# Kernel optimization log

Hardware: AMD Instinct MI355X
Metric: run time of the kernel (lower is better)

The kernel has to match this reference:

```python
import jax, jax.numpy as jnp
import numpy as np

X, Y, Z = 300, 300, 300
C = 16
N = 1048576
SCALE = 0.1


def _bilinear_sample(img, grid):
    # img: (C, H, W); grid: (M, 2) with (x, y) in [-1, 1]; align_corners=True
    _, H, W = img.shape
    ix = (grid[:, 0] + 1.0) * 0.5 * (W - 1)
    iy = (grid[:, 1] + 1.0) * 0.5 * (H - 1)
    ix0f = jnp.floor(ix)
    iy0f = jnp.floor(iy)
    wx = ix - ix0f  # (M,)
    wy = iy - iy0f
    ix0 = jnp.clip(ix0f.astype(jnp.int32), 0, W - 1)
    ix1 = jnp.clip(ix0 + 1, 0, W - 1)
    iy0 = jnp.clip(iy0f.astype(jnp.int32), 0, H - 1)
    iy1 = jnp.clip(iy0 + 1, 0, H - 1)
    # gathers give (C, M)
    v00 = img[:, iy0, ix0]
    v01 = img[:, iy0, ix1]
    v10 = img[:, iy1, ix0]
    v11 = img[:, iy1, ix1]
    return (v00 * (1 - wx) * (1 - wy) + v01 * wx * (1 - wy)
            + v10 * (1 - wx) * wy + v11 * wx * wy)  # (C, M)


def setup_inputs() -> dict:
    key = jax.random.key(0)
    ks = jax.random.split(key, 8)
    coords_plane = jax.random.uniform(ks[0], (3, 1, N, 1, 2), jnp.float32) * 2.0 - 1.0
    coords_line = jax.random.uniform(ks[1], (3, 1, N, 1, 2), jnp.float32) * 2.0 - 1.0
    plane_xy = SCALE * jax.random.normal(ks[2], (1, C, Y, X), jnp.float32)
    plane_yz = SCALE * jax.random.normal(ks[3], (1, C, Z, Y), jnp.float32)
    plane_xz = SCALE * jax.random.normal(ks[4], (1, C, Z, X), jnp.float32)
    line_x = SCALE * jax.random.normal(ks[5], (1, C, X, 1), jnp.float32)
    line_y = SCALE * jax.random.normal(ks[6], (1, C, Y, 1), jnp.float32)
    line_z = SCALE * jax.random.normal(ks[7], (1, C, Z, 1), jnp.float32)
    return {"coords_plane": coords_plane, "coords_line": coords_line,
            "plane_xy": plane_xy, "plane_yz": plane_yz, "plane_xz": plane_xz,
            "line_x": line_x, "line_y": line_y, "line_z": line_z}


def reference(coords_plane, coords_line, plane_xy, plane_yz, plane_xz,
              line_x, line_y, line_z):
    # coords_*[i]: (1, N, 1, 2) -> flatten to (N, 2)
    cp = coords_plane.reshape(3, -1, 2)
    cl = coords_line.reshape(3, -1, 2)
    f_xy = _bilinear_sample(plane_xy[0], cp[0])  # (C, N)
    f_yz = _bilinear_sample(plane_yz[0], cp[1])
    f_xz = _bilinear_sample(plane_xz[0], cp[2])
    f_x = _bilinear_sample(line_x[0], cl[0])
    f_y = _bilinear_sample(line_y[0], cl[1])
    f_z = _bilinear_sample(line_z[0], cl[2])
    out_x = (f_yz * f_x).T  # (N, C)
    out_y = (f_xz * f_y).T
    out_z = (f_xy * f_z).T
    return (out_x, out_y, out_z)
```

## Files before the change

kernel.cpp:

```cpp
#include <hip/hip_runtime.h>

#define DIMSZ 300
#define CCH   16
#define NPTS  1048576

typedef _Float16 half4 __attribute__((ext_vector_type(4)));
typedef float    fvec4 __attribute__((ext_vector_type(4)));
typedef float    fvec2 __attribute__((ext_vector_type(2)));

__device__ __forceinline__ fvec4 h2f(half4 h) {
    fvec4 r;
    r.x = (float)h[0]; r.y = (float)h[1]; r.z = (float)h[2]; r.w = (float)h[3];
    return r;
}

__global__ __launch_bounds__(256) void transpose_planes(
    const float* __restrict__ a, const float* __restrict__ b, const float* __restrict__ c,
    _Float16* __restrict__ ta, _Float16* __restrict__ tb, _Float16* __restrict__ tc)
{
    const int HW = DIMSZ * DIMSZ;
    const float* in  = (blockIdx.y == 0) ? a  : (blockIdx.y == 1) ? b  : c;
    _Float16*    out = (blockIdx.y == 0) ? ta : (blockIdx.y == 1) ? tb : tc;

    __shared__ float tile[64][CCH + 1];
    int pix0 = blockIdx.x * 64;
    int t = threadIdx.x;

    int p  = t & 63;
    int cg = t >> 6;
#pragma unroll
    for (int k = 0; k < 4; ++k) {
        int ch  = cg * 4 + k;
        int pix = pix0 + p;
        tile[p][ch] = (pix < HW) ? __builtin_nontemporal_load(&in[(size_t)ch * HW + pix]) : 0.f;
    }
    __syncthreads();

    int q  = t & 3;
    int pr = t >> 2;
    int pix = pix0 + pr;
    if (pix < HW) {
        half4 h;
        h[0] = (_Float16)tile[pr][q * 4 + 0];
        h[1] = (_Float16)tile[pr][q * 4 + 1];
        h[2] = (_Float16)tile[pr][q * 4 + 2];
        h[3] = (_Float16)tile[pr][q * 4 + 3];
        ((half4*)out)[(size_t)pix * 4 + q] = h;
    }
}

__global__ __launch_bounds__(256) void transpose_lines(
    const float* __restrict__ a, const float* __restrict__ b, const float* __restrict__ c,
    float* __restrict__ ta, float* __restrict__ tb, float* __restrict__ tc)
{
    const float* in  = (blockIdx.y == 0) ? a  : (blockIdx.y == 1) ? b  : c;
    float*       out = (blockIdx.y == 0) ? ta : (blockIdx.y == 1) ? tb : tc;
    for (int idx = threadIdx.x; idx < DIMSZ * CCH; idx += 256) {
        int p  = idx >> 4;
        int ch = idx & 15;
        out[idx] = in[ch * DIMSZ + p];
    }
}

template <int K>
__global__ __launch_bounds__(256) void td_plane(
    const float* __restrict__ coords_plane,
    const float* __restrict__ coords_line,
    const _Float16* __restrict__ ptex,
    const float* __restrict__ ltex,
    float* __restrict__ out)
{
    int gid = blockIdx.x * 256 + threadIdx.x;
    int i = gid >> 2;
    int q = gid & 3;
    if (i >= NPTS) return;

    constexpr int PC = (K == 0) ? 1 : (K == 1) ? 2 : 0;

    const fvec2* cp = (const fvec2*)coords_plane;
    const fvec2* cl = (const fvec2*)coords_line;
    fvec2 g   = __builtin_nontemporal_load(&cp[(size_t)PC * NPTS + i]);
    fvec2 glv = __builtin_nontemporal_load(&cl[(size_t)K * NPTS + i]);
    float gl  = glv.y;

    float ix = (g.x + 1.f) * 0.5f * (float)(DIMSZ - 1);
    float iy = (g.y + 1.f) * 0.5f * (float)(DIMSZ - 1);
    float ix0f = floorf(ix), iy0f = floorf(iy);
    float wx = ix - ix0f, wy = iy - iy0f;
    int ix0 = min(max((int)ix0f, 0), DIMSZ - 1);
    int ix1 = min(ix0 + 1, DIMSZ - 1);
    int iy0 = min(max((int)iy0f, 0), DIMSZ - 1);
    int iy1 = min(iy0 + 1, DIMSZ - 1);

    const half4* t4 = (const half4*)ptex;
    size_t r0 = (size_t)iy0 * DIMSZ;
    size_t r1 = (size_t)iy1 * DIMSZ;
    fvec4 v00 = h2f(t4[(r0 + ix0) * 4 + q]);
    fvec4 v01 = h2f(t4[(r0 + ix1) * 4 + q]);
    fvec4 v10 = h2f(t4[(r1 + ix0) * 4 + q]);
    fvec4 v11 = h2f(t4[(r1 + ix1) * 4 + q]);

    float w00 = (1.f - wx) * (1.f - wy);
    float w01 = wx * (1.f - wy);
    float w10 = (1.f - wx) * wy;
    float w11 = wx * wy;

    fvec4 f = v00 * w00 + v01 * w01 + v10 * w10 + v11 * w11;

    float lyv = (gl + 1.f) * 0.5f * (float)(DIMSZ - 1);
    float ly0f = floorf(lyv);
    float wl = lyv - ly0f;
    int l0 = min(max((int)ly0f, 0), DIMSZ - 1);
    int l1 = min(l0 + 1, DIMSZ - 1);

    const fvec4* l4 = (const fvec4*)ltex;
    fvec4 u0 = l4[(size_t)l0 * 4 + q];
    fvec4 u1 = l4[(size_t)l1 * 4 + q];
    fvec4 fl = u0 * (1.f - wl) + u1 * wl;

    fvec4* out4 = (fvec4*)out;
    __builtin_nontemporal_store(f * fl,
                                &out4[(size_t)K * NPTS * 4 + (size_t)i * 4 + q]);
}

__global__ __launch_bounds__(256) void td_fallback(
    const float* __restrict__ coords_plane,
    const float* __restrict__ coords_line,
    const float* __restrict__ pxy, const float* __restrict__ pyz,
    const float* __restrict__ pxz,
    const float* __restrict__ lx, const float* __restrict__ ly,
    const float* __restrict__ lz,
    float* __restrict__ out)
{
    int gid = blockIdx.x * 256 + threadIdx.x;
    int i = gid >> 2;
    int q = gid & 3;
    if (i >= NPTS) return;

    const fvec2* cp = (const fvec2*)coords_plane;
    const fvec2* cl = (const fvec2*)coords_line;

    fvec4* out4 = (fvec4*)out;
    const float* planes[3] = {pyz, pxz, pxy};
    const float* lines[3]  = {lx, ly, lz};
    const int    pcs[3]    = {1, 2, 0};

#pragma unroll
    for (int k = 0; k < 3; ++k) {
        fvec2 g  = cp[(size_t)pcs[k] * NPTS + i];
        float gl = cl[(size_t)k * NPTS + i].y;

        float ix = (g.x + 1.f) * 0.5f * (float)(DIMSZ - 1);
        float iy = (g.y + 1.f) * 0.5f * (float)(DIMSZ - 1);
        float ix0f = floorf(ix), iy0f = floorf(iy);
        float wx = ix - ix0f, wy = iy - iy0f;
        int ix0 = min(max((int)ix0f, 0), DIMSZ - 1);
        int ix1 = min(ix0 + 1, DIMSZ - 1);
        int iy0 = min(max((int)iy0f, 0), DIMSZ - 1);
        int iy1 = min(iy0 + 1, DIMSZ - 1);
        float w00 = (1.f - wx) * (1.f - wy), w01 = wx * (1.f - wy);
        float w10 = (1.f - wx) * wy,         w11 = wx * wy;

        float lyv = (gl + 1.f) * 0.5f * (float)(DIMSZ - 1);
        float ly0f = floorf(lyv);
        float wl = lyv - ly0f;
        int l0 = min(max((int)ly0f, 0), DIMSZ - 1);
        int l1 = min(l0 + 1, DIMSZ - 1);

        const float* P = planes[k];
        const float* L = lines[k];
        size_t hw = (size_t)DIMSZ * DIMSZ;
        int b00 = iy0 * DIMSZ + ix0, b01 = iy0 * DIMSZ + ix1;
        int b10 = iy1 * DIMSZ + ix0, b11 = iy1 * DIMSZ + ix1;
        fvec4 r;
#pragma unroll
        for (int j = 0; j < 4; ++j) {
            size_t cb = (size_t)(q * 4 + j) * hw;
            float fp = P[cb + b00] * w00 + P[cb + b01] * w01 +
                       P[cb + b10] * w10 + P[cb + b11] * w11;
            size_t lb = (size_t)(q * 4 + j) * DIMSZ;
            float flv = L[lb + l0] * (1.f - wl) + L[lb + l1] * wl;
            r[j] = fp * flv;
        }
        out4[(size_t)k * NPTS * 4 + (size_t)i * 4 + q] = r;
    }
}

extern "C" void kernel_launch(void* const* d_in, const int* in_sizes, int n_in,
                              void* d_out, int out_size, void* d_ws, size_t ws_size,
                              hipStream_t stream)
{
    const float* coords_plane = (const float*)d_in[0];
    const float* coords_line  = (const float*)d_in[1];
    const float* pxy = (const float*)d_in[2];
    const float* pyz = (const float*)d_in[3];
    const float* pxz = (const float*)d_in[4];
    const float* lx  = (const float*)d_in[5];
    const float* ly  = (const float*)d_in[6];
    const float* lz  = (const float*)d_in[7];
    float* out = (float*)d_out;

    const size_t planeH = (size_t)DIMSZ * DIMSZ * CCH;
    const size_t lineF  = (size_t)DIMSZ * CCH;
    const size_t needBytes = 3 * planeH * sizeof(_Float16) + 3 * lineF * sizeof(float);

    const int blocks = (NPTS * 4 + 255) / 256;

    if (ws_size >= needBytes) {
        char* w = (char*)d_ws;
        _Float16* txy = (_Float16*)w;
        _Float16* tyz = txy + planeH;
        _Float16* txz = tyz + planeH;
        float* tlx = (float*)(w + 3 * planeH * sizeof(_Float16));
        float* tly = tlx + lineF;
        float* tlz = tly + lineF;

        dim3 gp((DIMSZ * DIMSZ + 63) / 64, 3);
        transpose_planes<<<gp, 256, 0, stream>>>(pxy, pyz, pxz, txy, tyz, txz);
        dim3 gl(1, 3);
        transpose_lines<<<gl, 256, 0, stream>>>(lx, ly, lz, tlx, tly, tlz);

        td_plane<0><<<blocks, 256, 0, stream>>>(coords_plane, coords_line, tyz, tlx, out);
        td_plane<1><<<blocks, 256, 0, stream>>>(coords_plane, coords_line, txz, tly, out);
        td_plane<2><<<blocks, 256, 0, stream>>>(coords_plane, coords_line, txy, tlz, out);
    } else {
        td_fallback<<<blocks, 256, 0, stream>>>(coords_plane, coords_line,
                                                pxy, pyz, pxz, lx, ly, lz, out);
    }
}
```

Before: 133.2 us.

## Fuse three per-plane sampling kernels into one launch with LDS-staged line textures

Replaces the three templated per-plane kernels with a single kernel whose block index selects the plane/line pair, cutting two launches and the tail gaps between them. Each block copies its 300x16 line texture (about 19 KB) into shared memory and reads the line samples from there instead of global memory. Non-temporal loads and stores are also dropped in favour of ordinary cached accesses. The per-block LDS fill and barrier add fixed overhead to every one of the 49k blocks and may reduce occupancy.

Result: no change. 132.7 us (-0.4%).

```diff
diff --git a/kernel.cpp b/kernel.cpp
--- a/kernel.cpp
+++ b/kernel.cpp
@@ -3,6 +3,7 @@
 #define DIMSZ 300
 #define CCH   16
 #define NPTS  1048576
+#define BLOCKS_PER_K 16384
 
 typedef _Float16 half4 __attribute__((ext_vector_type(4)));
 typedef float    fvec4 __attribute__((ext_vector_type(4)));
@@ -32,7 +33,7 @@
     for (int k = 0; k < 4; ++k) {
         int ch  = cg * 4 + k;
         int pix = pix0 + p;
-        tile[p][ch] = (pix < HW) ? __builtin_nontemporal_load(&in[(size_t)ch * HW + pix]) : 0.f;
+        tile[p][ch] = (pix < HW) ? in[(size_t)ch * HW + pix] : 0.f;
     }
     __syncthreads();
 
@@ -62,26 +63,38 @@
     }
 }
 
-template <int K>
-__global__ __launch_bounds__(256) void td_plane(
+__global__ __launch_bounds__(256) void td_all(
     const float* __restrict__ coords_plane,
     const float* __restrict__ coords_line,
-    const _Float16* __restrict__ ptex,
-    const float* __restrict__ ltex,
+    const _Float16* __restrict__ tyz, const _Float16* __restrict__ txz,
+    const _Float16* __restrict__ txy,
+    const float* __restrict__ tlx, const float* __restrict__ tly,
+    const float* __restrict__ tlz,
     float* __restrict__ out)
 {
-    int gid = blockIdx.x * 256 + threadIdx.x;
+    const int K = blockIdx.x >> 14;
+    const int b = blockIdx.x & (BLOCKS_PER_K - 1);
+
+    const _Float16* ptex = (K == 0) ? tyz : (K == 1) ? txz : txy;
+    const float*    ltex = (K == 0) ? tlx : (K == 1) ? tly : tlz;
+    const int PC = (K == 0) ? 1 : (K == 1) ? 2 : 0;
+
+    __shared__ fvec4 lline[DIMSZ * 4];
+    {
+        const fvec4* l4 = (const fvec4*)ltex;
+        for (int idx = threadIdx.x; idx < DIMSZ * 4; idx += 256)
+            lline[idx] = l4[idx];
+    }
+    __syncthreads();
+
+    int gid = b * 256 + threadIdx.x;
     int i = gid >> 2;
     int q = gid & 3;
-    if (i >= NPTS) return;
-
-    constexpr int PC = (K == 0) ? 1 : (K == 1) ? 2 : 0;
 
     const fvec2* cp = (const fvec2*)coords_plane;
     const fvec2* cl = (const fvec2*)coords_line;
-    fvec2 g   = __builtin_nontemporal_load(&cp[(size_t)PC * NPTS + i]);
-    fvec2 glv = __builtin_nontemporal_load(&cl[(size_t)K * NPTS + i]);
-    float gl  = glv.y;
+    fvec2 g   = cp[(size_t)PC * NPTS + i];
+    float gl  = cl[(size_t)K * NPTS + i].y;
 
     float ix = (g.x + 1.f) * 0.5f * (float)(DIMSZ - 1);
     float iy = (g.y + 1.f) * 0.5f * (float)(DIMSZ - 1);
@@ -113,14 +126,12 @@
     int l0 = min(max((int)ly0f, 0), DIMSZ - 1);
     int l1 = min(l0 + 1, DIMSZ - 1);
 
-    const fvec4* l4 = (const fvec4*)ltex;
-    fvec4 u0 = l4[(size_t)l0 * 4 + q];
-    fvec4 u1 = l4[(size_t)l1 * 4 + q];
+    fvec4 u0 = lline[l0 * 4 + q];
+    fvec4 u1 = lline[l1 * 4 + q];
     fvec4 fl = u0 * (1.f - wl) + u1 * wl;
 
     fvec4* out4 = (fvec4*)out;
-    __builtin_nontemporal_store(f * fl,
-                                &out4[(size_t)K * NPTS * 4 + (size_t)i * 4 + q]);
+    out4[(size_t)K * NPTS * 4 + (size_t)i * 4 + q] = f * fl;
 }
 
 __global__ __launch_bounds__(256) void td_fallback(
@@ -204,8 +215,6 @@
     const size_t lineF  = (size_t)DIMSZ * CCH;
     const size_t needBytes = 3 * planeH * sizeof(_Float16) + 3 * lineF * sizeof(float);
 
-    const int blocks = (NPTS * 4 + 255) / 256;
-
     if (ws_size >= needBytes) {
         char* w = (char*)d_ws;
         _Float16* txy = (_Float16*)w;
@@ -220,10 +229,10 @@
         dim3 gl(1, 3);
         transpose_lines<<<gl, 256, 0, stream>>>(lx, ly, lz, tlx, tly, tlz);
 
-        td_plane<0><<<blocks, 256, 0, stream>>>(coords_plane, coords_line, tyz, tlx, out);
-        td_plane<1><<<blocks, 256, 0, stream>>>(coords_plane, coords_line, txz, tly, out);
-        td_plane<2><<<blocks, 256, 0, stream>>>(coords_plane, coords_line, txy, tlz, out);
+        td_all<<<3 * BLOCKS_PER_K, 256, 0, stream>>>(coords_plane, coords_line,
+                                                     tyz, txz, txy, tlx, tly, tlz, out);
     } else {
+        const int blocks = (NPTS * 4 + 255) / 256;
         td_fallback<<<blocks, 256, 0, stream>>>(coords_plane, coords_line,
                                                 pxy, pyz, pxz, lx, ly, lz, out);
     }
```

## Pack horizontal texel pairs into fp16 plane layout and interpolate via lane shuffles

Applied to the files above, without the earlier changes.

The transposed fp16 plane is rebuilt so each pixel entry holds its own 16 channels followed by the right neighbour's 16 channels (32 halves per pixel). A lane then needs two 16-byte loads, rows iy0 and iy1, instead of four 8-byte gathers. The x-interpolation partner values are exchanged between adjacent lanes with shuffles. This doubles the workspace texture footprint and adds cross-lane shuffles, trading cache capacity for fewer gather requests. Nontemporal hints on the coordinate loads and output stores are also dropped.

New measurement: 132.6 us. About the same (-0.5%).

```diff
diff --git a/kernel.cpp b/kernel.cpp
--- a/kernel.cpp
+++ b/kernel.cpp
@@ -4,13 +4,15 @@
 #define CCH   16
 #define NPTS  1048576
 
-typedef _Float16 half4 __attribute__((ext_vector_type(4)));
+typedef _Float16 half8 __attribute__((ext_vector_type(8)));
+typedef float    fvec8 __attribute__((ext_vector_type(8)));
 typedef float    fvec4 __attribute__((ext_vector_type(4)));
 typedef float    fvec2 __attribute__((ext_vector_type(2)));
 
-__device__ __forceinline__ fvec4 h2f(half4 h) {
-    fvec4 r;
-    r.x = (float)h[0]; r.y = (float)h[1]; r.z = (float)h[2]; r.w = (float)h[3];
+__device__ __forceinline__ fvec8 h2f8(half8 h) {
+    fvec8 r;
+#pragma unroll
+    for (int j = 0; j < 8; ++j) r[j] = (float)h[j];
     return r;
 }
 
@@ -32,20 +34,26 @@
     for (int k = 0; k < 4; ++k) {
         int ch  = cg * 4 + k;
         int pix = pix0 + p;
-        tile[p][ch] = (pix < HW) ? __builtin_nontemporal_load(&in[(size_t)ch * HW + pix]) : 0.f;
+        tile[p][ch] = (pix < HW) ? in[(size_t)ch * HW + pix] : 0.f;
     }
     __syncthreads();
 
-    int q  = t & 3;
-    int pr = t >> 2;
-    int pix = pix0 + pr;
+    int q    = t & 3;
+    int h    = q & 1;
+    int role = q >> 1;
+    int pr   = t >> 2;
+    int pix  = pix0 + pr;
     if (pix < HW) {
-        half4 h;
-        h[0] = (_Float16)tile[pr][q * 4 + 0];
-        h[1] = (_Float16)tile[pr][q * 4 + 1];
-        h[2] = (_Float16)tile[pr][q * 4 + 2];
-        h[3] = (_Float16)tile[pr][q * 4 + 3];
-        ((half4*)out)[(size_t)pix * 4 + q] = h;
+        int x = pix % DIMSZ;
+        half8 v;
+#pragma unroll
+        for (int j = 0; j < 8; ++j) v[j] = (_Float16)tile[pr][h * 8 + j];
+        half8* o8 = (half8*)out;
+        if (role == 0) {
+            if (x <= DIMSZ - 2) o8[(size_t)pix * 4 + h] = v;
+        } else {
+            if (x >= 1)         o8[(size_t)(pix - 1) * 4 + 2 + h] = v;
+        }
     }
 }
 
@@ -79,33 +87,37 @@
 
     const fvec2* cp = (const fvec2*)coords_plane;
     const fvec2* cl = (const fvec2*)coords_line;
-    fvec2 g   = __builtin_nontemporal_load(&cp[(size_t)PC * NPTS + i]);
-    fvec2 glv = __builtin_nontemporal_load(&cl[(size_t)K * NPTS + i]);
-    float gl  = glv.y;
+    fvec2 g  = cp[(size_t)PC * NPTS + i];
+    float gl = cl[(size_t)K * NPTS + i].y;
 
     float ix = (g.x + 1.f) * 0.5f * (float)(DIMSZ - 1);
     float iy = (g.y + 1.f) * 0.5f * (float)(DIMSZ - 1);
     float ix0f = floorf(ix), iy0f = floorf(iy);
     float wx = ix - ix0f, wy = iy - iy0f;
-    int ix0 = min(max((int)ix0f, 0), DIMSZ - 1);
-    int ix1 = min(ix0 + 1, DIMSZ - 1);
+    int ix0 = min(max((int)ix0f, 0), DIMSZ - 2);
     int iy0 = min(max((int)iy0f, 0), DIMSZ - 1);
     int iy1 = min(iy0 + 1, DIMSZ - 1);
 
-    const half4* t4 = (const half4*)ptex;
-    size_t r0 = (size_t)iy0 * DIMSZ;
-    size_t r1 = (size_t)iy1 * DIMSZ;
-    fvec4 v00 = h2f(t4[(r0 + ix0) * 4 + q]);
-    fvec4 v01 = h2f(t4[(r0 + ix1) * 4 + q]);
-    fvec4 v10 = h2f(t4[(r1 + ix0) * 4 + q]);
-    fvec4 v11 = h2f(t4[(r1 + ix1) * 4 + q]);
-
-    float w00 = (1.f - wx) * (1.f - wy);
-    float w01 = wx * (1.f - wy);
-    float w10 = (1.f - wx) * wy;
-    float w11 = wx * wy;
-
-    fvec4 f = v00 * w00 + v01 * w01 + v10 * w10 + v11 * w11;
+    const half8* t8 = (const half8*)ptex;
+    int chunk = ((q & 1) << 1) | (q >> 1);
+    half8 g0 = t8[((size_t)iy0 * DIMSZ + ix0) * 4 + chunk];
+    half8 g1 = t8[((size_t)iy1 * DIMSZ + ix0) * 4 + chunk];
+
+    fvec8 a0 = h2f8(g0);
+    fvec8 a1 = h2f8(g1);
+    fvec8 ty = a0 * (1.f - wy) + a1 * wy;
+
+    fvec8 tu;
+#pragma unroll
+    for (int j = 0; j < 8; ++j) tu[j] = __shfl_xor(ty[j], 1);
+
+    bool hiPix = (q & 1) != 0;
+    fvec8 fx = hiPix ? (tu * (1.f - wx) + ty * wx)
+                     : (ty * (1.f - wx) + tu * wx);
+
+    fvec4 lo = {fx[0], fx[1], fx[2], fx[3]};
+    fvec4 hi = {fx[4], fx[5], fx[6], fx[7]};
+    fvec4 fq = (q & 1) ? hi : lo;
 
     float lyv = (gl + 1.f) * 0.5f * (float)(DIMSZ - 1);
     float ly0f = floorf(lyv);
@@ -119,8 +131,7 @@
     fvec4 fl = u0 * (1.f - wl) + u1 * wl;
 
     fvec4* out4 = (fvec4*)out;
-    __builtin_nontemporal_store(f * fl,
-                                &out4[(size_t)K * NPTS * 4 + (size_t)i * 4 + q]);
+    out4[(size_t)K * NPTS * 4 + (size_t)i * 4 + q] = fq * fl;
 }
 
 __global__ __launch_bounds__(256) void td_fallback(
@@ -200,11 +211,9 @@
     const float* lz  = (const float*)d_in[7];
     float* out = (float*)d_out;
 
-    const size_t planeH = (size_t)DIMSZ * DIMSZ * CCH;
+    const size_t planeH = (size_t)DIMSZ * DIMSZ * 32;
     const size_t lineF  = (size_t)DIMSZ * CCH;
     const size_t needBytes = 3 * planeH * sizeof(_Float16) + 3 * lineF * sizeof(float);
-
-    const int blocks = (NPTS * 4 + 255) / 256;
 
     if (ws_size >= needBytes) {
         char* w = (char*)d_ws;
@@ -220,10 +229,12 @@
         dim3 gl(1, 3);
         transpose_lines<<<gl, 256, 0, stream>>>(lx, ly, lz, tlx, tly, tlz);
 
+        const int blocks = (NPTS * 4 + 255) / 256;
         td_plane<0><<<blocks, 256, 0, stream>>>(coords_plane, coords_line, tyz, tlx, out);
         td_plane<1><<<blocks, 256, 0, stream>>>(coords_plane, coords_line, txz, tly, out);
         td_plane<2><<<blocks, 256, 0, stream>>>(coords_plane, coords_line, txy, tlz, out);
     } else {
+        const int blocks = (NPTS * 4 + 255) / 256;
         td_fallback<<<blocks, 256, 0, stream>>>(coords_plane, coords_line,
                                                 pxy, pyz, pxz, lx, ly, lz, out);
     }
```
